# Performance work log

Hardware: AMD Instinct MI355X
Metric: run time of the kernel (lower is better)

## Reference

```python
import jax, jax.numpy as jnp
import numpy as np

EMBED = 512
HEADS = 8
DIM_HEAD = 64          # embed_dim // 8
LANDMARKS = 256        # embed_dim // 2
PINV_ITERS = 6
RES_K = 33             # nystrom residual_conv_kernel default
SCALE = DIM_HEAD ** -0.5


def layer_norm(x, g, b, eps=1e-5):
    mu = x.mean(-1, keepdims=True)
    var = ((x - mu) ** 2).mean(-1, keepdims=True)
    return (x - mu) / jnp.sqrt(var + eps) * g + b


def moore_penrose_pinv(x, iters=PINV_ITERS):
    # iterative Moore-Penrose pseudo-inverse (lucidrains nystrom-attention)
    ax = jnp.abs(x)
    z = jnp.swapaxes(x, -1, -2) / (ax.sum(-1).max() * ax.sum(-2).max())
    I = jnp.eye(x.shape[-1], dtype=x.dtype)
    for _ in range(iters):
        xz = x @ z
        z = 0.25 * z @ (13. * I - xz @ (15. * I - xz @ (7. * I - xz)))
    return z


def nystrom_attention(x, w_qkv, w_out, b_out, res_k):
    b, n, _ = x.shape
    m = LANDMARKS
    pad = (m - n % m) % m
    xp = jnp.pad(x, ((0, 0), (pad, 0), (0, 0)))  # left-pad like F.pad(..., padding, 0)
    np_ = n + pad
    qkv = (xp @ w_qkv).reshape(b, np_, 3, HEADS, DIM_HEAD)
    q = qkv[:, :, 0].transpose(0, 2, 1, 3) * SCALE   # [b,h,np,dh]
    k = qkv[:, :, 1].transpose(0, 2, 1, 3)
    v = qkv[:, :, 2].transpose(0, 2, 1, 3)
    l = np_ // m
    q_l = q.reshape(b, HEADS, m, l, DIM_HEAD).mean(3)  # [b,h,m,dh]
    k_l = k.reshape(b, HEADS, m, l, DIM_HEAD).mean(3)
    attn1 = jax.nn.softmax(jnp.einsum('bhid,bhjd->bhij', q, k_l), -1)    # [b,h,np,m]
    attn2 = jax.nn.softmax(jnp.einsum('bhid,bhjd->bhij', q_l, k_l), -1)  # [b,h,m,m]
    attn3 = jax.nn.softmax(jnp.einsum('bhid,bhjd->bhij', q_l, k), -1)    # [b,h,m,np]
    out = (attn1 @ moore_penrose_pinv(attn2)) @ (attn3 @ v)              # [b,h,np,dh]
    # depthwise residual conv over the sequence dim, per head (shared across dh)
    v_c = v.transpose(0, 3, 1, 2).reshape(b * DIM_HEAD, HEADS, np_)
    res = jax.lax.conv_general_dilated(
        v_c, res_k[:, None, :], (1,), [(RES_K // 2, RES_K // 2)],
        dimension_numbers=('NCH', 'OIH', 'NCH'), feature_group_count=HEADS)
    out = out + res.reshape(b, DIM_HEAD, HEADS, np_).transpose(0, 2, 3, 1)
    out = out.transpose(0, 2, 1, 3).reshape(b, np_, HEADS * DIM_HEAD)
    out = out @ w_out + b_out
    return out[:, -n:]  # drop left padding


def dwconv2d(x, w, b, k):
    # x: [B,C,H,W], w: [C,1,k,k] depthwise
    y = jax.lax.conv_general_dilated(
        x, w, (1, 1), [(k // 2, k // 2)] * 2,
        dimension_numbers=('NCHW', 'OIHW', 'NCHW'), feature_group_count=x.shape[1])
    return y + b[None, :, None, None]


def ppeg(x, H, W, w7, b7, w5, b5, w3, b3):
    B, _, C = x.shape
    cls_tok, feat = x[:, :1], x[:, 1:]
    f = feat.transpose(0, 2, 1).reshape(B, C, H, W)
    y = f + dwconv2d(f, w7, b7, 7) + dwconv2d(f, w5, b5, 5) + dwconv2d(f, w3, b3, 3)
    y = y.reshape(B, C, H * W).transpose(0, 2, 1)
    return jnp.concatenate([cls_tok, y], axis=1)


def reference(h, w_fc1, b_fc1, cls_token,
              ln1_g, ln1_b, qkv1_w, out1_w, out1_b, res1_k,
              conv7_w, conv7_b, conv5_w, conv5_b, conv3_w, conv3_b,
              ln2_g, ln2_b, qkv2_w, out2_w, out2_b, res2_k,
              lnf_g, lnf_b):
    h = jax.nn.relu(h @ w_fc1 + b_fc1)                 # [B,N,512]
    B, N, C = h.shape
    _H = int(np.ceil(np.sqrt(N)))
    add = _H * _H - N
    h = jnp.concatenate([h, h[:, :add]], axis=1)       # square padding
    h = jnp.concatenate([jnp.broadcast_to(cls_token, (B, 1, C)), h], axis=1)
    h = h + nystrom_attention(layer_norm(h, ln1_g, ln1_b), qkv1_w, out1_w, out1_b, res1_k)
    h = ppeg(h, _H, _H, conv7_w, conv7_b, conv5_w, conv5_b, conv3_w, conv3_b)
    h = h + nystrom_attention(layer_norm(h, ln2_g, ln2_b), qkv2_w, out2_w, out2_b, res2_k)
    return layer_norm(h, lnf_g, lnf_b)[:, 0]           # [B,512]


def setup_inputs() -> dict:
    key = jax.random.key(0)
    ks = jax.random.split(key, 24)
    B, N, IN_DIM = 2, 4096, 1024
    w = lambda k, shape, s=0.02: jax.random.normal(k, shape, jnp.float32) * s
    z = lambda shape: jnp.zeros(shape, jnp.float32)
    o = lambda shape: jnp.ones(shape, jnp.float32)
    return {
        'h': jax.random.normal(ks[0], (B, N, IN_DIM), jnp.float32),
        'w_fc1': w(ks[1], (IN_DIM, EMBED)), 'b_fc1': z((EMBED,)),
        'cls_token': w(ks[2], (1, 1, EMBED)),
        'ln1_g': o((EMBED,)), 'ln1_b': z((EMBED,)),
        'qkv1_w': w(ks[3], (EMBED, 3 * HEADS * DIM_HEAD)),
        'out1_w': w(ks[4], (HEADS * DIM_HEAD, EMBED)), 'out1_b': z((EMBED,)),
        'res1_k': w(ks[5], (HEADS, RES_K), 0.1),
        'conv7_w': w(ks[6], (EMBED, 1, 7, 7), 0.05), 'conv7_b': z((EMBED,)),
        'conv5_w': w(ks[7], (EMBED, 1, 5, 5), 0.05), 'conv5_b': z((EMBED,)),
        'conv3_w': w(ks[8], (EMBED, 1, 3, 3), 0.05), 'conv3_b': z((EMBED,)),
        'ln2_g': o((EMBED,)), 'ln2_b': z((EMBED,)),
        'qkv2_w': w(ks[9], (EMBED, 3 * HEADS * DIM_HEAD)),
        'out2_w': w(ks[10], (HEADS * DIM_HEAD, EMBED)), 'out2_b': z((EMBED,)),
        'res2_k': w(ks[11], (HEADS, RES_K), 0.1),
        'lnf_g': o((EMBED,)), 'lnf_b': z((EMBED,)),
    }
```

## Files before the change

### kernel.cpp

```cpp
#include <hip/hip_runtime.h>
#include <hip/hip_bf16.h>

#define HEADS 8
#define DH 64
#define EMB 512
#define NP 4352
#define NTOK 4097
#define PADF 255
#define LM 256
#define SCALE 0.125f

typedef __attribute__((ext_vector_type(8))) short bf8;
typedef __attribute__((ext_vector_type(4))) float f4;
typedef __attribute__((ext_vector_type(8))) unsigned short us8;
typedef __attribute__((ext_vector_type(4))) unsigned short us4;
typedef unsigned short u16;

__device__ __forceinline__ u16 f2b(float f){
  union { float f; unsigned u; } x; x.f = f;
  unsigned r = x.u + 0x7fffu + ((x.u>>16)&1u);
  return (u16)(r>>16);
}
__device__ __forceinline__ float b2f(u16 h){
  union { unsigned u; float f; } x; x.u = ((unsigned)h)<<16;
  return x.f;
}

__device__ __forceinline__ void gload_lds(const u16* g, u16* l){
  __builtin_amdgcn_global_load_lds((const __attribute__((address_space(1))) void*)g,
                                   (__attribute__((address_space(3))) void*)l, 16, 0, 0);
}

template<int MODE>
__global__ __launch_bounds__(256)
void k_g128(const u16* __restrict__ A, const u16* __restrict__ B,
            float* __restrict__ C, u16* __restrict__ C16,
            int K, int lda, int ldb, int ldc,
            long sAb, long sAh, long sBb, long sBh, long sCb, long sCh, int nh,
            float alpha, const float* __restrict__ bias, int relu, int rowoff,
            int nx, int ksplit)
{
  int z = blockIdx.z;
  const u16* Ab = A + (long)(z/nh)*sAb + (long)(z%nh)*sAh;
  const u16* Bb = B + (long)(z/nh)*sBb + (long)(z%nh)*sBh;
  long cb = (long)(z/nh)*sCb + (long)(z%nh)*sCh;
  int bx = blockIdx.x % nx, kc = blockIdx.x / nx;
  int m0 = blockIdx.y*128, n0 = bx*128;
  int klen = K/ksplit, kbeg = kc*klen, nch = klen/32;
  __shared__ u16 As[2][4096];
  __shared__ u16 Bs[2][4096];
  int tid=threadIdx.x, w=tid>>6, lane=tid&63, q=lane>>4, lr=lane&15;
  int wrow=(w>>1)*64, wcol=(w&1)*64;
  int srow = tid>>2, scol = (tid&3)*8;
  const u16* ga  = Ab + (long)(m0+srow)*lda + kbeg + scol;
  const u16* ga2 = Ab + (long)(m0+64+srow)*lda + kbeg + scol;
  const u16* gb  = Bb + (long)(n0+srow)*ldb + kbeg + scol;
  const u16* gb2 = Bb + (long)(n0+64+srow)*ldb + kbeg + scol;
  int lo = srow*32 + scol;
  f4 acc[4][4] = {};
  auto stage = [&](int r, int c){
    gload_lds(ga  + c*32, &As[r][lo]);
    gload_lds(ga2 + c*32, &As[r][2048+lo]);
    gload_lds(gb  + c*32, &Bs[r][lo]);
    gload_lds(gb2 + c*32, &Bs[r][2048+lo]);
  };
  auto compute = [&](int r){
    bf8 af[4], bfr[4];
    #pragma unroll
    for(int rr=0;rr<4;rr++) af[rr]  = *(const bf8*)&As[r][(wrow + rr*16 + lr)*32 + q*8];
    #pragma unroll
    for(int t=0;t<4;t++) bfr[t] = *(const bf8*)&Bs[r][(wcol + t*16 + lr)*32 + q*8];
    #pragma unroll
    for(int rr=0;rr<4;rr++)
      #pragma unroll
      for(int t=0;t<4;t++)
        acc[rr][t] = __builtin_amdgcn_mfma_f32_16x16x32_bf16(af[rr], bfr[t], acc[rr][t], 0,0,0);
  };
  stage(0,0);
  __syncthreads();
  for(int c=1;c<nch;c++){
    stage(c&1, c);
    compute((c-1)&1);
    __syncthreads();
  }
  compute((nch-1)&1);
  #pragma unroll
  for(int r=0;r<4;r++){
    #pragma unroll
    for(int t=0;t<4;t++){
      #pragma unroll
      for(int e=0;e<4;e++){
        int gm = m0 + wrow + r*16 + q*4 + e;
        int gn = n0 + wcol + t*16 + lr;
        float v = acc[r][t][e]*alpha;
        if(MODE==4){
          if(bias && kc==0) v += bias[gn];
          if(gm>=rowoff) atomicAdd(&C[cb + (long)(gm-rowoff)*ldc + gn], v);
        } else {
          if(bias) v += bias[gn];
          if(relu) v = fmaxf(v,0.f);
          if(MODE==0) C[cb + (long)gm*ldc + gn] = v;
          else if(MODE==2) C16[cb + (long)gm*ldc + gn] = f2b(v);
          else { if(gm>=rowoff) C[cb + (long)(gm-rowoff)*ldc + gn] += v; }
        }
      }
    }
  }
}

template<int MODE>
__global__ __launch_bounds__(256)
void k_g64(const u16* __restrict__ A, const u16* __restrict__ B,
           float* __restrict__ C, u16* __restrict__ C16,
           int K, int lda, int ldb, int ldc,
           long sAb, long sAh, long sBb, long sBh, long sCb, long sCh, int nh,
           float alpha, const float* __restrict__ bias, int rowoff, int moff,
           int nx, int ksplit)
{
  int z = blockIdx.z;
  const u16* Ab = A + (long)(z/nh)*sAb + (long)(z%nh)*sAh;
  const u16* Bb = B + (long)(z/nh)*sBb + (long)(z%nh)*sBh;
  long cb = (long)(z/nh)*sCb + (long)(z%nh)*sCh;
  int bx = blockIdx.x % nx, kc = blockIdx.x / nx;
  int m0 = blockIdx.y*64 + moff, n0 = bx*64;
  int klen = K/ksplit, kbeg = kc*klen, nch = klen/32;
  __shared__ u16 As[2][2048];
  __shared__ u16 Bs[2][2048];
  int tid=threadIdx.x, w=tid>>6, lane=tid&63, q=lane>>4, lr=lane&15;
  int srow = tid>>2, scol = (tid&3)*8;
  const u16* ga = Ab + (long)(m0+srow)*lda + kbeg + scol;
  const u16* gb = Bb + (long)(n0+srow)*ldb + kbeg + scol;
  int lo = srow*32 + scol;
  f4 acc[4] = {};
  auto stage = [&](int r, int c){
    gload_lds(ga + c*32, &As[r][lo]);
    gload_lds(gb + c*32, &Bs[r][lo]);
  };
  auto compute = [&](int r){
    bf8 af = *(const bf8*)&As[r][(w*16 + lr)*32 + q*8];
    #pragma unroll
    for(int t=0;t<4;t++){
      bf8 bfr = *(const bf8*)&Bs[r][(t*16 + lr)*32 + q*8];
      acc[t] = __builtin_amdgcn_mfma_f32_16x16x32_bf16(af, bfr, acc[t], 0,0,0);
    }
  };
  stage(0,0);
  __syncthreads();
  for(int c=1;c<nch;c++){
    stage(c&1, c);
    compute((c-1)&1);
    __syncthreads();
  }
  compute((nch-1)&1);
  #pragma unroll
  for(int t=0;t<4;t++){
    #pragma unroll
    for(int e=0;e<4;e++){
      int gm = m0 + w*16 + q*4 + e;
      int gn = n0 + t*16 + lr;
      float v = acc[t][e]*alpha;
      if(MODE==0) C[cb + (long)gm*ldc + gn] = v;
      else if(MODE==2) C16[cb + (long)gm*ldc + gn] = f2b(v);
      else if(MODE==3) atomicAdd(&C[cb + (long)gm*ldc + gn], v);
      else if(MODE==5){
        v += bias[gn];
        if(gm>=rowoff) C[cb + (long)(gm-rowoff)*ldc + gn] += v;
      }
    }
  }
}

__global__ __launch_bounds__(256)
void k_pg3(const u16* __restrict__ Ah, const u16* __restrict__ Al,
           const u16* __restrict__ Bh, const u16* __restrict__ Bl,
           u16* __restrict__ Oh, u16* __restrict__ Ol, float na, float nd,
           u16* __restrict__ TOh, u16* __restrict__ TOl, float ta, float td)
{
  long zo = (long)blockIdx.z*65536;
  int m0 = blockIdx.y*32, n0 = blockIdx.x*64;
  __shared__ u16 S[2][6144];
  int tid=threadIdx.x, w=tid>>6, lane=tid&63, q=lane>>4, lr=lane&15;
  int t2 = tid & 127;
  const u16* srcA = (tid<128 ? Ah : Al) + zo + (long)(m0 + (t2>>2))*256 + (t2&3)*8;
  const u16* srcBh = Bh + zo + (long)(n0 + (tid>>2))*256 + (tid&3)*8;
  const u16* srcBl = Bl + zo + (long)(n0 + (tid>>2))*256 + (tid&3)*8;
  f4 acc[2] = {};
  auto stage = [&](int r, int c){
    gload_lds(srcA  + c*32, &S[r][tid*8]);
    gload_lds(srcBh + c*32, &S[r][2048 + tid*8]);
    gload_lds(srcBl + c*32, &S[r][4096 + tid*8]);
  };
  int mrow = (w>>1)*16 + lr;
  auto compute = [&](int r){
    bf8 ah = *(const bf8*)&S[r][mrow*32 + q*8];
    bf8 al = *(const bf8*)&S[r][1024 + mrow*32 + q*8];
    #pragma unroll
    for(int t=0;t<2;t++){
      int nrow = (w&1)*32 + t*16 + lr;
      bf8 bh = *(const bf8*)&S[r][2048 + nrow*32 + q*8];
      bf8 bl = *(const bf8*)&S[r][4096 + nrow*32 + q*8];
      acc[t] = __builtin_amdgcn_mfma_f32_16x16x32_bf16(ah, bh, acc[t], 0,0,0);
      acc[t] = __builtin_amdgcn_mfma_f32_16x16x32_bf16(ah, bl, acc[t], 0,0,0);
      acc[t] = __builtin_amdgcn_mfma_f32_16x16x32_bf16(al, bh, acc[t], 0,0,0);
    }
  };
  stage(0,0);
  __syncthreads();
  #pragma unroll
  for(int c=1;c<8;c++){
    stage(c&1, c);
    compute((c-1)&1);
    __syncthreads();
  }
  compute(1);
  #pragma unroll
  for(int t=0;t<2;t++){
    int gn = n0 + (w&1)*32 + t*16 + lr;
    if(Oh){
      #pragma unroll
      for(int r=0;r<4;r++){
        int gm = m0 + (w>>1)*16 + q*4 + r;
        float v = na*acc[t][r] + ((gm==gn)?nd:0.f);
        u16 h = f2b(v);
        long o = zo + (long)gm*256 + gn;
        Oh[o] = h; Ol[o] = f2b(v - b2f(h));
      }
    }
    if(TOh){
      us4 th, tl;
      #pragma unroll
      for(int r=0;r<4;r++){
        int gm = m0 + (w>>1)*16 + q*4 + r;
        float v = ta*acc[t][r] + ((gm==gn)?td:0.f);
        u16 h = f2b(v);
        th[r] = h; tl[r] = f2b(v - b2f(h));
      }
      long o = zo + (long)gn*256 + (m0 + (w>>1)*16 + q*4);
      *(us4*)&TOh[o] = th; *(us4*)&TOl[o] = tl;
    }
  }
}

__global__ __launch_bounds__(128)
void k_att3(const u16* __restrict__ qkv16, const u16* __restrict__ ql,
            const u16* __restrict__ vT, float* __restrict__ partO,
            float* __restrict__ pm, float* __restrict__ pl)
{
  int kc = blockIdx.x, jt = blockIdx.y, z = blockIdx.z;
  int b = z>>3, h = z&7;
  __shared__ u16 SQ[32*64];
  __shared__ u16 SK[2][64*64];
  __shared__ u16 SV[2][64*64];
  __shared__ u16 SP[32*64];
  int tid=threadIdx.x, w=tid>>6, lane=tid&63, q=lane>>4, lr=lane&15;
  const u16* kb = qkv16 + (long)b*NP*1536 + 512 + h*64;
  const u16* vb = vT + (long)z*64*NP;
  int t00 = kc*1088;
  {
    const u16* qb = ql + (long)z*16384 + jt*32*64;
    #pragma unroll
    for(int p=0;p<2;p++){ int idx = tid + p*128; gload_lds(qb + idx*8, &SQ[idx*8]); }
  }
  auto stageKV = [&](int r, int i){
    int t0 = t00 + i*64;
    #pragma unroll
    for(int p=0;p<4;p++){
      int idx = tid + p*128; int row = idx>>3, c8 = (idx&7)*8;
      gload_lds(kb + (long)(t0+row)*1536 + c8, &SK[r][idx*8]);
      gload_lds(vb + (long)row*NP + t0 + c8, &SV[r][idx*8]);
    }
  };
  stageKV(0,0);
  __syncthreads();
  bf8 af0 = *(const bf8*)&SQ[(w*16+lr)*64 + q*8];
  bf8 af1 = *(const bf8*)&SQ[(w*16+lr)*64 + 32 + q*8];
  f4 o[4] = {};
  float m[4] = {-3e38f,-3e38f,-3e38f,-3e38f};
  float l[4] = {0.f,0.f,0.f,0.f};
  for(int i=0;i<17;i++){
    int cur = i&1;
    if(i<16) stageKV(cur^1, i+1);
    f4 s[4] = {};
    #pragma unroll
    for(int t=0;t<4;t++){
      bf8 b0 = *(const bf8*)&SK[cur][(t*16+lr)*64 + q*8];
      bf8 b1 = *(const bf8*)&SK[cur][(t*16+lr)*64 + 32 + q*8];
      s[t] = __builtin_amdgcn_mfma_f32_16x16x32_bf16(af0, b0, s[t], 0,0,0);
      s[t] = __builtin_amdgcn_mfma_f32_16x16x32_bf16(af1, b1, s[t], 0,0,0);
    }
    float tm[4];
    #pragma unroll
    for(int e=0;e<4;e++) tm[e] = fmaxf(fmaxf(s[0][e],s[1][e]), fmaxf(s[2][e],s[3][e]));
    #pragma unroll
    for(int sh=1; sh<16; sh<<=1)
      #pragma unroll
      for(int e=0;e<4;e++) tm[e] = fmaxf(tm[e], __shfl_xor(tm[e], sh));
    float rs[4];
    #pragma unroll
    for(int e=0;e<4;e++){
      float mn = fmaxf(m[e], tm[e]);
      float sc = expf(m[e]-mn);
      m[e] = mn;
      l[e] *= sc;
      rs[e] = 0.f;
      o[0][e]*=sc; o[1][e]*=sc; o[2][e]*=sc; o[3][e]*=sc;
    }
    #pragma unroll
    for(int t=0;t<4;t++)
      #pragma unroll
      for(int e=0;e<4;e++){
        float p = expf(s[t][e]-m[e]);
        rs[e] += p;
        SP[(w*16+q*4+e)*64 + t*16+lr] = f2b(p);
      }
    #pragma unroll
    for(int sh=1; sh<16; sh<<=1)
      #pragma unroll
      for(int e=0;e<4;e++) rs[e] += __shfl_xor(rs[e], sh);
    #pragma unroll
    for(int e=0;e<4;e++) l[e] += rs[e];
    #pragma unroll
    for(int ks=0;ks<2;ks++){
      bf8 pa = *(const bf8*)&SP[(w*16+lr)*64 + ks*32 + q*8];
      #pragma unroll
      for(int t2=0;t2<4;t2++){
        bf8 vv = *(const bf8*)&SV[cur][(t2*16+lr)*64 + ks*32 + q*8];
        o[t2] = __builtin_amdgcn_mfma_f32_16x16x32_bf16(pa, vv, o[t2], 0,0,0);
      }
    }
    __syncthreads();
  }
  long pb = (long)(z*4+kc)*256 + jt*32 + w*16;
  #pragma unroll
  for(int e=0;e<4;e++){
    int jg = q*4+e;
    #pragma unroll
    for(int t2=0;t2<4;t2++)
      partO[(pb + jg)*64 + t2*16 + lr] = o[t2][e];
    if(lr==0){ pm[pb + jg] = m[e]; pl[pb + jg] = l[e]; }
  }
}

__global__ __launch_bounds__(128)
void k_mrg3(const float* __restrict__ partO, const float* __restrict__ pm,
            const float* __restrict__ pl, u16* __restrict__ avbT16)
{
  int jq = blockIdx.x, z = blockIdx.y, tid = threadIdx.x;
  __shared__ float wk[64][4];
  __shared__ u16 T[64][66];
  if(tid < 64){
    int j = jq*64 + tid;
    float mm[4], ll[4];
    #pragma unroll
    for(int kc=0;kc<4;kc++){ mm[kc]=pm[(z*4+kc)*256 + j]; ll[kc]=pl[(z*4+kc)*256 + j]; }
    float M = fmaxf(fmaxf(mm[0],mm[1]),fmaxf(mm[2],mm[3]));
    float e0=expf(mm[0]-M), e1=expf(mm[1]-M), e2=expf(mm[2]-M), e3=expf(mm[3]-M);
    float inv = 1.f/(ll[0]*e0+ll[1]*e1+ll[2]*e2+ll[3]*e3);
    wk[tid][0]=e0*inv; wk[tid][1]=e1*inv; wk[tid][2]=e2*inv; wk[tid][3]=e3*inv;
  }
  __syncthreads();
  float acc[32];
  #pragma unroll
  for(int p=0;p<32;p++) acc[p]=0.f;
  for(int kc=0;kc<4;kc++){
    long base = ((long)(z*4+kc)*256 + jq*64)*64;
    #pragma unroll
    for(int p=0;p<32;p++){
      int idx = tid + p*128;
      acc[p] += wk[idx>>6][kc]*partO[base + idx];
    }
  }
  #pragma unroll
  for(int p=0;p<32;p++){ int idx = tid + p*128; T[idx&63][idx>>6] = f2b(acc[p]); }
  __syncthreads();
  int d = tid>>1, jh = (tid&1)*32;
  u16* dst = avbT16 + (long)(z*64+d)*256 + jq*64 + jh;
  #pragma unroll
  for(int c=0;c<4;c++){
    us8 vv;
    #pragma unroll
    for(int u=0;u<8;u++) vv[u] = T[d][jh + c*8 + u];
    *(us8*)&dst[c*8] = vv;
  }
}

__global__ __launch_bounds__(256)
void k_att1(const u16* __restrict__ qkv16, const u16* __restrict__ kl,
            const u16* __restrict__ zavT, float* __restrict__ Qc)
{
  int z = blockIdx.y, b = z>>3, h = z&7;
  int m0 = blockIdx.x*64;
  __shared__ u16 SQ[64*64];
  __shared__ u16 SKL[256*64];
  __shared__ u16 SZV[64*256];
  int tid=threadIdx.x, w=tid>>6, lane=tid&63, q=lane>>4, lr=lane&15;
  {
    const u16* qb = qkv16 + (long)b*NP*1536 + h*64;
    #pragma unroll
    for(int p=0;p<2;p++){
      int idx = tid + p*256; int row = idx>>3, c8 = (idx&7)*8;
      gload_lds(qb + (long)(m0+row)*1536 + c8, &SQ[row*64 + c8]);
    }
    const u16* kb = kl + (long)z*16384;
    #pragma unroll
    for(int p=0;p<8;p++){
      int idx = tid + p*256; int row = idx>>3, c8 = (idx&7)*8;
      gload_lds(kb + row*64 + c8, &SKL[row*64 + c8]);
    }
    const u16* zb = zavT + (long)z*16384;
    #pragma unroll
    for(int p=0;p<8;p++){
      int idx = tid + p*256; int row = idx>>5, c8 = (idx&31)*8;
      gload_lds(zb + row*256 + c8, &SZV[row*256 + c8]);
    }
  }
  __syncthreads();
  f4 acc[16] = {};
  {
    bf8 af0 = *(const bf8*)&SQ[(w*16+lr)*64 + q*8];
    bf8 af1 = *(const bf8*)&SQ[(w*16+lr)*64 + 32 + q*8];
    #pragma unroll
    for(int t=0;t<16;t++){
      bf8 b0 = *(const bf8*)&SKL[(t*16+lr)*64 + q*8];
      bf8 b1 = *(const bf8*)&SKL[(t*16+lr)*64 + 32 + q*8];
      acc[t] = __builtin_amdgcn_mfma_f32_16x16x32_bf16(af0, b0, acc[t], 0,0,0);
      acc[t] = __builtin_amdgcn_mfma_f32_16x16x32_bf16(af1, b1, acc[t], 0,0,0);
    }
  }
  float mx[4] = {-1e30f,-1e30f,-1e30f,-1e30f};
  #pragma unroll
  for(int t=0;t<16;t++)
    #pragma unroll
    for(int e=0;e<4;e++) mx[e] = fmaxf(mx[e], acc[t][e]*SCALE);
  #pragma unroll
  for(int s=1;s<16;s<<=1)
    #pragma unroll
    for(int e=0;e<4;e++) mx[e] = fmaxf(mx[e], __shfl_xor(mx[e], s));
  float sm[4] = {0.f,0.f,0.f,0.f};
  #pragma unroll
  for(int t=0;t<16;t++)
    #pragma unroll
    for(int e=0;e<4;e++){ float p = expf(acc[t][e]*SCALE - mx[e]); acc[t][e]=p; sm[e]+=p; }
  #pragma unroll
  for(int s=1;s<16;s<<=1)
    #pragma unroll
    for(int e=0;e<4;e++) sm[e] += __shfl_xor(sm[e], s);
  float inv[4];
  #pragma unroll
  for(int e=0;e<4;e++) inv[e] = 1.f/sm[e];
  __syncthreads();
  u16* PS = SKL;
  #pragma unroll
  for(int t=0;t<16;t++)
    #pragma unroll
    for(int e=0;e<4;e++)
      PS[(w*16 + q*4 + e)*256 + t*16 + lr] = f2b(acc[t][e]*inv[e]);
  __syncthreads();
  f4 acc2[4] = {};
  #pragma unroll
  for(int ks=0;ks<8;ks++){
    bf8 af = *(const bf8*)&PS[(w*16+lr)*256 + ks*32 + q*8];
    #pragma unroll
    for(int t=0;t<4;t++){
      bf8 bf_ = *(const bf8*)&SZV[(t*16+lr)*256 + ks*32 + q*8];
      acc2[t] = __builtin_amdgcn_mfma_f32_16x16x32_bf16(af, bf_, acc2[t], 0,0,0);
    }
  }
  #pragma unroll
  for(int t=0;t<4;t++)
    #pragma unroll
    for(int r=0;r<4;r++){
      int gm = m0 + w*16 + q*4 + r;
      int gd = t*16 + lr;
      Qc[((long)b*NP + gm)*512 + h*64 + gd] = acc2[t][r];
    }
}

__global__ __launch_bounds__(256)
void k_smw32(float* __restrict__ X){
  long row = (long)blockIdx.x*4 + (threadIdx.x>>6);
  int lane = threadIdx.x & 63;
  float* p = X + row*256;
  float4 v = *(float4*)&p[lane*4];
  float m = fmaxf(fmaxf(v.x,v.y),fmaxf(v.z,v.w));
  for(int s=32;s;s>>=1) m = fmaxf(m, __shfl_xor(m, s));
  float e0=expf(v.x-m), e1=expf(v.y-m), e2=expf(v.z-m), e3=expf(v.w-m);
  float sum = e0+e1+e2+e3;
  for(int s=32;s;s>>=1) sum += __shfl_xor(sum, s);
  float inv = 1.f/sum;
  float4 o = {e0*inv, e1*inv, e2*inv, e3*inv};
  *(float4*)&p[lane*4] = o;
}

__global__ void k_wT(const float* __restrict__ in, u16* __restrict__ out, int K, int N){
  int n0=blockIdx.x*32, k0=blockIdx.y*32, tid=threadIdx.x;
  __shared__ float T[32][33];
  int lr=tid&31, lc=tid>>5;
  #pragma unroll
  for(int p=0;p<4;p++) T[lc+8*p][lr] = in[(long)(k0+lc+8*p)*N + n0+lr];
  __syncthreads();
  #pragma unroll
  for(int p=0;p<4;p++) out[(long)(n0+lc+8*p)*K + k0+lr] = f2b(T[lr][lc+8*p]);
}

__global__ __launch_bounds__(256)
void k_vT(const u16* __restrict__ qkv16, u16* __restrict__ vT){
  int t0=blockIdx.x*64, h=blockIdx.y, b=blockIdx.z, tid=threadIdx.x;
  __shared__ u16 T[64][72];
  const u16* src = qkv16 + (long)b*NP*1536 + 1024 + h*64;
  for(int s=0;s<2;s++){
    int idx=tid+s*256; int row=idx>>3, c8=(idx&7)*8;
    *(us8*)&T[row][c8] = *(const us8*)&src[(long)(t0+row)*1536 + c8];
  }
  __syncthreads();
  u16* dst = vT + ((long)(b*8+h)*64)*NP;
  int d = tid>>2, j0=(tid&3)*16;
  us8 v0,v1;
  #pragma unroll
  for(int jj=0;jj<8;jj++){ v0[jj]=T[j0+jj][d]; v1[jj]=T[j0+8+jj][d]; }
  *(us8*)&dst[(long)d*NP + t0 + j0]     = v0;
  *(us8*)&dst[(long)d*NP + t0 + j0 + 8] = v1;
}

__global__ void k_cvt16(const float* __restrict__ in, u16* __restrict__ out, long n){
  long i = (long)blockIdx.x*256 + threadIdx.x;
  if(i<n) out[i] = f2b(in[i]);
}

__global__ void k_cls(const float* __restrict__ cls, float* __restrict__ seq){
  int b = blockIdx.x;
  seq[(long)b*NTOK*EMB + threadIdx.x] = cls[threadIdx.x];
}

__global__ void k_ln_pad(const float* __restrict__ seq, u16* __restrict__ xp,
                         const float* __restrict__ g, const float* __restrict__ bb){
  int b = blockIdx.y, i = blockIdx.x, tid = threadIdx.x;
  u16* out = xp + ((long)b*NP + i)*EMB;
  if(i < PADF){ out[tid]=0; out[tid+256]=0; return; }
  const float* x = seq + ((long)b*NTOK + (i-PADF))*EMB;
  float v0 = x[tid], v1 = x[tid+256];
  __shared__ float red[256];
  red[tid]=v0+v1; __syncthreads();
  for(int s=128;s>0;s>>=1){ if(tid<s) red[tid]+=red[tid+s]; __syncthreads(); }
  float mu = red[0]*(1.0f/512.0f); __syncthreads();
  float d0=v0-mu, d1=v1-mu;
  red[tid]=d0*d0+d1*d1; __syncthreads();
  for(int s=128;s>0;s>>=1){ if(tid<s) red[tid]+=red[tid+s]; __syncthreads(); }
  float rstd = rsqrtf(red[0]*(1.0f/512.0f) + 1e-5f);
  out[tid]     = f2b(d0*rstd*g[tid]     + bb[tid]);
  out[tid+256] = f2b(d1*rstd*g[tid+256] + bb[tid+256]);
}

__global__ void k_landmarks(const u16* __restrict__ qkv, u16* __restrict__ q_l, u16* __restrict__ k_l){
  int j = blockIdx.x, h = blockIdx.y, b = blockIdx.z, d = threadIdx.x;
  const u16* base = qkv + (long)b*NP*1536 + h*64 + d;
  float sq=0.f, sk=0.f;
  for(int l=0;l<17;l++){
    long row = (long)(j*17+l)*1536;
    sq += b2f(base[row]);
    sk += b2f(base[row+512]);
  }
  long o = (((long)b*HEADS + h)*LM + j)*DH + d;
  q_l[o] = f2b(sq * (SCALE/17.0f));
  k_l[o] = f2b(sk * (1.0f/17.0f));
}

__global__ void k_pinv_norm(const float* __restrict__ A2, float* __restrict__ rmax, float* __restrict__ cmax){
  int z = blockIdx.x, tid = threadIdx.x;
  const float* X = A2 + (long)z*65536;
  float rs=0.f, cs=0.f;
  for(int j=0;j<256;j++){ rs += fabsf(X[tid*256+j]); cs += fabsf(X[j*256+tid]); }
  __shared__ float r1[256], r2[256];
  r1[tid]=rs; r2[tid]=cs; __syncthreads();
  for(int s=128;s>0;s>>=1){ if(tid<s){ r1[tid]=fmaxf(r1[tid],r1[tid+s]); r2[tid]=fmaxf(r2[tid],r2[tid+s]); } __syncthreads(); }
  if(tid==0){ rmax[z]=r1[0]; cmax[z]=r2[0]; }
}

__global__ void k_pair_init(const float* __restrict__ att2,
    const float* __restrict__ rmax, const float* __restrict__ cmax,
    u16* __restrict__ Xh, u16* __restrict__ Xl,
    u16* __restrict__ Zh, u16* __restrict__ Zl,
    u16* __restrict__ Zth, u16* __restrict__ Ztl)
{
  long zo = (long)blockIdx.z*65536;
  int i0 = blockIdx.y*64, j0 = blockIdx.x*64;
  float rm=0.f, cm=0.f;
  for(int t=0;t<16;t++){ rm=fmaxf(rm,rmax[t]); cm=fmaxf(cm,cmax[t]); }
  float inv = 1.0f/(rm*cm);
  __shared__ float T[64][68];
  int tid = threadIdx.x;
  int li = tid>>2, jc = (tid&3)*16;
  #pragma unroll
  for(int u=0;u<4;u++){
    float4 v = *(const float4*)&att2[zo + (long)(i0+li)*256 + j0 + jc + u*4];
    T[li][jc+u*4]=v.x; T[li][jc+u*4+1]=v.y; T[li][jc+u*4+2]=v.z; T[li][jc+u*4+3]=v.w;
    long o = zo + (long)(i0+li)*256 + j0 + jc + u*4;
    float vv[4] = {v.x,v.y,v.z,v.w};
    us4 xh, xl, zth, ztl;
    #pragma unroll
    for(int c=0;c<4;c++){
      u16 h = f2b(vv[c]); xh[c]=h; xl[c]=f2b(vv[c]-b2f(h));
      float zt = vv[c]*inv;
      u16 h2 = f2b(zt); zth[c]=h2; ztl[c]=f2b(zt-b2f(h2));
    }
    *(us4*)&Xh[o]=xh; *(us4*)&Xl[o]=xl; *(us4*)&Zth[o]=zth; *(us4*)&Ztl[o]=ztl;
  }
  __syncthreads();
  int lj = tid>>2, ic = (tid&3)*16;
  #pragma unroll
  for(int r=0;r<16;r++){
    float x = T[ic+r][lj]*inv;
    u16 h = f2b(x);
    long o = zo + (long)(j0+lj)*256 + i0 + ic + r;
    Zh[o]=h; Zl[o]=f2b(x-b2f(h));
  }
}

__global__ __launch_bounds__(256)
void k_rconv(const u16* __restrict__ qkv16, const float* __restrict__ resk,
             const float* __restrict__ Qin, u16* __restrict__ Qo16){
  int t0 = blockIdx.x*64, h = blockIdx.y, b = blockIdx.z;
  __shared__ float V[96*64];
  const u16* vb = qkv16 + (long)b*NP*1536 + 1024 + h*64;
  int tid = threadIdx.x;
  #pragma unroll
  for(int s=0;s<3;s++){
    int idx = tid + s*256;
    int row = idx>>3, c8 = (idx&7)*8;
    int p = t0 - 16 + row;
    if(p>=0 && p<NP){
      us8 v = *(const us8*)&vb[(long)p*1536 + c8];
      #pragma unroll
      for(int jj=0;jj<8;jj++) V[row*64+c8+jj] = b2f(v[jj]);
    } else {
      #pragma unroll
      for(int jj=0;jj<8;jj++) V[row*64+c8+jj] = 0.f;
    }
  }
  __syncthreads();
  int d = tid&63, lt = (tid>>6)*16;
  float acc[16] = {};
  #pragma unroll
  for(int s=0;s<48;s++){
    float val = V[(lt+s)*64 + d];
    #pragma unroll
    for(int j=0;j<16;j++){
      int tap = s - j;
      if(tap>=0 && tap<33) acc[j] += resk[h*33+tap]*val;
    }
  }
  #pragma unroll
  for(int j=0;j<16;j++){
    long idx = ((long)b*NP + t0 + lt + j)*EMB + h*64 + d;
    Qo16[idx] = f2b(Qin[idx] + acc[j]);
  }
}

__global__ __launch_bounds__(256)
void k_ppeg(const float* __restrict__ seq, float* __restrict__ out,
    const float* __restrict__ w7,const float* __restrict__ b7,
    const float* __restrict__ w5,const float* __restrict__ b5,
    const float* __restrict__ w3,const float* __restrict__ b3){
  int b = blockIdx.z, cg = blockIdx.y;
  int rp = blockIdx.x>>1, xs = blockIdx.x&1;
  int ch0 = cg*64;
  __shared__ float s7[64*49], s5[64*25], s3[64*9], sbias[64];
  int tid = threadIdx.x;
  for(int i=tid;i<64*49;i+=256) s7[i] = w7[ch0*49+i];
  for(int i=tid;i<64*25;i+=256) s5[i] = w5[ch0*25+i];
  for(int i=tid;i<64*9;i+=256)  s3[i] = w3[ch0*9+i];
  if(tid<64) sbias[tid] = b7[ch0+tid]+b5[ch0+tid]+b3[ch0+tid];
  if(cg==0 && blockIdx.x==0){
    out[(long)b*NTOK*EMB + tid]       = seq[(long)b*NTOK*EMB + tid];
    out[(long)b*NTOK*EMB + 256 + tid] = seq[(long)b*NTOK*EMB + 256 + tid];
  }
  __syncthreads();
  int c = tid & 63;
  int y = rp*4 + (tid>>6);
  const float* sbase = seq + (long)b*NTOK*EMB + EMB + (ch0 + c);
  float* obase = out + (long)b*NTOK*EMB + EMB + (ch0 + c);
  const float* W7 = &s7[c*49];
  const float* W5 = &s5[c*25];
  const float* W3 = &s3[c*9];
  float bsum = sbias[c];
  for(int xc=0;xc<4;xc++){
    int xb = xs*32 + xc*8;
    float acc[8];
    #pragma unroll
    for(int j=0;j<8;j++) acc[j] = sbase[(long)(y*64+xb+j)*EMB] + bsum;
    #pragma unroll
    for(int dy=-3;dy<=3;dy++){
      int yy = y+dy;
      if(yy<0||yy>=64) continue;
      float v[14];
      #pragma unroll
      for(int u=0;u<14;u++){
        int xx = xb + u - 3;
        v[u] = (xx>=0 && xx<64) ? sbase[(long)(yy*64+xx)*EMB] : 0.f;
      }
      #pragma unroll
      for(int dx=-3;dx<=3;dx++){
        float wsum = W7[(dy+3)*7+(dx+3)];
        if(dy>=-2&&dy<=2&&dx>=-2&&dx<=2) wsum += W5[(dy+2)*5+(dx+2)];
        if(dy>=-1&&dy<=1&&dx>=-1&&dx<=1) wsum += W3[(dy+1)*3+(dx+1)];
        #pragma unroll
        for(int j=0;j<8;j++) acc[j] += v[j+dx+3]*wsum;
      }
    }
    #pragma unroll
    for(int j=0;j<8;j++) obase[(long)(y*64+xb+j)*EMB] = acc[j];
  }
}

__global__ void k_final_ln(const float* __restrict__ seq, const float* __restrict__ g,
                           const float* __restrict__ bb, float* __restrict__ out){
  int b = blockIdx.x, tid = threadIdx.x;
  const float* x = seq + (long)b*NTOK*EMB;
  float v0 = x[tid], v1 = x[tid+256];
  __shared__ float red[256];
  red[tid]=v0+v1; __syncthreads();
  for(int s=128;s>0;s>>=1){ if(tid<s) red[tid]+=red[tid+s]; __syncthreads(); }
  float mu = red[0]*(1.0f/512.0f); __syncthreads();
  float d0=v0-mu, d1=v1-mu;
  red[tid]=d0*d0+d1*d1; __syncthreads();
  for(int s=128;s>0;s>>=1){ if(tid<s) red[tid]+=red[tid+s]; __syncthreads(); }
  float rstd = rsqrtf(red[0]*(1.0f/512.0f) + 1e-5f);
  out[b*512+tid]     = d0*rstd*g[tid]     + bb[tid];
  out[b*512+tid+256] = d1*rstd*g[tid+256] + bb[tid+256];
}

extern "C" void kernel_launch(void* const* d_in, const int* in_sizes, int n_in,
                              void* d_out, int out_size, void* d_ws, size_t ws_size,
                              hipStream_t stream) {
  const float* in[24];
  for(int i=0;i<24;i++) in[i] = (const float*)d_in[i];

  float* W = (float*)d_ws;
  size_t off = 0;
  float* seqA = W+off; off += 4195328;
  float* seqB = W+off; off += 4195328;
  float* att2 = W+off; off += 1048576;
  float* Qc   = W+off; off += 4456448;
  float* partO= W+off; off += 1048576;
  float* pm   = W+off; off += 16384;
  float* pl   = W+off; off += 16384;
  u16* xpb    = (u16*)(W+off); off += 2228224;
  u16* qkvb16 = (u16*)(W+off); off += 6684672;
  u16* vT16   = (u16*)(W+off); off += 2228224;
  u16* q_l16  = (u16*)(W+off); off += 131072;
  u16* k_l16  = (u16*)(W+off); off += 131072;
  u16* avbT16 = (u16*)(W+off); off += 131072;
  u16* zavT16 = (u16*)(W+off); off += 131072;
  u16* Qc16   = (u16*)(W+off); off += 2228224;
  u16* qkvwT1 = (u16*)(W+off); off += 393216;
  u16* qkvwT2 = (u16*)(W+off); off += 393216;
  u16* outwT1 = (u16*)(W+off); off += 131072;
  u16* outwT2 = (u16*)(W+off); off += 131072;
  u16* pairs  = (u16*)(W+off); off += 9437184;
  float* rmax = W+off; off += 16;
  float* cmax = W+off; off += 16;
  if (ws_size < off*sizeof(float)) return;

  u16* h16   = pairs;
  u16* wfc1T = pairs + 8388608;

  const long PB = 1048576;
  u16 *Xh=pairs, *Xl=pairs+PB;
  u16 *Z0h=pairs+2*PB, *Z0l=pairs+3*PB, *Z0th=pairs+4*PB, *Z0tl=pairs+5*PB;
  u16 *Z1h=pairs+6*PB, *Z1l=pairs+7*PB, *Z1th=pairs+8*PB, *Z1tl=pairs+9*PB;
  u16 *Ph=pairs+10*PB, *Pl=pairs+11*PB;
  u16 *Tth=pairs+12*PB, *Ttl=pairs+13*PB;
  u16 *Uth=pairs+14*PB, *Utl=pairs+15*PB;
  u16 *Vth=pairs+16*PB, *Vtl=pairs+17*PB;

  k_cvt16<<<32768,256,0,stream>>>(in[0], h16, 8388608L);
  k_wT<<<dim3(16,32),256,0,stream>>>(in[1],  wfc1T, 1024, 512);
  k_wT<<<dim3(48,16),256,0,stream>>>(in[6],  qkvwT1, 512, 1536);
  k_wT<<<dim3(48,16),256,0,stream>>>(in[18], qkvwT2, 512, 1536);
  k_wT<<<dim3(16,16),256,0,stream>>>(in[7],  outwT1, 512, 512);
  k_wT<<<dim3(16,16),256,0,stream>>>(in[19], outwT2, 512, 512);

  k_g128<0><<<dim3(4,32,2),256,0,stream>>>(h16, wfc1T, seqA+EMB, nullptr,
      1024, 1024,1024,512, 4194304L,0, 0,0, (long)NTOK*EMB,0, 1, 1.0f, in[2], 1, 0, 4, 1);
  k_cls<<<2,512,0,stream>>>(in[3], seqA);

  auto attention = [&](float* seq, const float* lng,const float* lnb,
                       const u16* qkvwT, const u16* outwT, const float* outb, const float* resk){
    k_ln_pad<<<dim3(NP,2),256,0,stream>>>(seq, xpb, lng, lnb);
    k_g128<2><<<dim3(12,34,2),256,0,stream>>>(xpb, qkvwT, nullptr, qkvb16,
        512, 512,512,1536, (long)NP*512,0, 0,0, (long)NP*1536,0, 1, 1.0f, nullptr, 0, 0, 12, 1);
    k_landmarks<<<dim3(LM,HEADS,2),64,0,stream>>>(qkvb16, q_l16, k_l16);
    k_vT<<<dim3(68,8,2),256,0,stream>>>(qkvb16, vT16);
    k_g128<0><<<dim3(2,2,16),256,0,stream>>>(q_l16, k_l16, att2, nullptr,
        64, 64,64,256, 0,16384, 0,16384, 0,65536, 16, 1.0f, nullptr, 0, 0, 2, 1);
    k_smw32<<<1024,256,0,stream>>>(att2);
    k_pinv_norm<<<16,256,0,stream>>>(att2, rmax, cmax);
    k_pair_init<<<dim3(4,4,16),256,0,stream>>>(att2, rmax, cmax, Xh,Xl, Z0h,Z0l, Z0th,Z0tl);
    dim3 pgrid(4,8,16);
    for(int it=0; it<6; it++){
      u16 *Zh_=(it&1)?Z1h:Z0h, *Zl_=(it&1)?Z1l:Z0l, *Zth_=(it&1)?Z1th:Z0th, *Ztl_=(it&1)?Z1tl:Z0tl;
      u16 *Nh_=(it&1)?Z0h:Z1h, *Nl_=(it&1)?Z0l:Z1l, *Nth_=(it&1)?Z0th:Z1th, *Ntl_=(it&1)?Z0tl:Z1tl;
      k_pg3<<<pgrid,256,0,stream>>>(Xh,Xl, Zth_,Ztl_, Ph,Pl,1.0f,0.f, Tth,Ttl,-1.0f,7.f);
      k_pg3<<<pgrid,256,0,stream>>>(Ph,Pl, Tth,Ttl, nullptr,nullptr,0.f,0.f, Uth,Utl,-1.0f,15.f);
      k_pg3<<<pgrid,256,0,stream>>>(Ph,Pl, Uth,Utl, nullptr,nullptr,0.f,0.f, Vth,Vtl,-1.0f,13.f);
      if(it<5) k_pg3<<<pgrid,256,0,stream>>>(Zh_,Zl_, Vth,Vtl, Nh_,Nl_,0.25f,0.f, Nth_,Ntl_,0.25f,0.f);
      else     k_pg3<<<pgrid,256,0,stream>>>(Zh_,Zl_, Vth,Vtl, Nh_,Nl_,0.25f,0.f, nullptr,nullptr,0.f,0.f);
    }
    k_att3<<<dim3(4,8,16),128,0,stream>>>(qkvb16, q_l16, vT16, partO, pm, pl);
    k_mrg3<<<dim3(4,16),128,0,stream>>>(partO, pm, pl, avbT16);
    k_g64<2><<<dim3(4,1,16),256,0,stream>>>(avbT16, Z0h, nullptr, zavT16,
        256, 256,256,256, 0,16384L, 0,65536L, 0,16384L, 16, 1.0f, nullptr, 0, 0, 4, 1);
    k_att1<<<dim3(68,16),256,0,stream>>>(qkvb16, k_l16, zavT16, Qc);
    k_rconv<<<dim3(68,8,2),256,0,stream>>>(qkvb16, resk, Qc, Qc16);
    k_g64<5><<<dim3(8,65,2),256,0,stream>>>(Qc16, outwT, seq, nullptr,
        512, 512,512,512, (long)NP*512,0, 0,0, (long)NTOK*EMB,0, 1, 1.0f, outb, PADF, 192, 8, 1);
  };

  attention(seqA, in[4], in[5], qkvwT1, outwT1, in[8], in[9]);
  k_ppeg<<<dim3(32,8,2),256,0,stream>>>(seqA, seqB, in[10],in[11],in[12],in[13],in[14],in[15]);
  attention(seqB, in[16], in[17], qkvwT2, outwT2, in[20], in[21]);
  k_final_ln<<<2,256,0,stream>>>(seqB, in[22], in[23], (float*)d_out);
}
```

Before: 1.025 ms.

## Split attn3 into more key chunks, widen blocks, swizzle LDS

The landmark-to-token attention (attn3 @ v) now splits the 4352-token key dimension into 17 chunks of 256 instead of 4 chunks of 1088. Each block processes 64 query landmarks with 256 threads instead of 32 with 128, giving 1088 blocks instead of 512 and a much shorter serial loop per block. LDS tiles for Q, K, V and P use an XOR swizzle on 8-element groups to avoid bank conflicts. The merge kernel is rewritten to combine 17 partial softmax results with finer 16-row tiles, at the cost of a much larger partial-output buffer and more merge traffic.

```diff
diff --git a/kernel.cpp b/kernel.cpp
--- a/kernel.cpp
+++ b/kernel.cpp
@@ -241,50 +241,55 @@
   }
 }
 
-__global__ __launch_bounds__(128)
+__global__ __launch_bounds__(256)
 void k_att3(const u16* __restrict__ qkv16, const u16* __restrict__ ql,
             const u16* __restrict__ vT, float* __restrict__ partO,
             float* __restrict__ pm, float* __restrict__ pl)
 {
   int kc = blockIdx.x, jt = blockIdx.y, z = blockIdx.z;
   int b = z>>3, h = z&7;
-  __shared__ u16 SQ[32*64];
+  __shared__ u16 SQ[64*64];
   __shared__ u16 SK[2][64*64];
   __shared__ u16 SV[2][64*64];
-  __shared__ u16 SP[32*64];
+  __shared__ u16 SP[64*64];
   int tid=threadIdx.x, w=tid>>6, lane=tid&63, q=lane>>4, lr=lane&15;
   const u16* kb = qkv16 + (long)b*NP*1536 + 512 + h*64;
   const u16* vb = vT + (long)z*64*NP;
-  int t00 = kc*1088;
+  int t00 = kc*256;
   {
-    const u16* qb = ql + (long)z*16384 + jt*32*64;
-    #pragma unroll
-    for(int p=0;p<2;p++){ int idx = tid + p*128; gload_lds(qb + idx*8, &SQ[idx*8]); }
+    const u16* qb = ql + (long)z*16384 + jt*64*64;
+    #pragma unroll
+    for(int p=0;p<2;p++){
+      int idx = tid + p*256; int row = idx>>3; int js = ((idx&7)^(row&7))<<3;
+      gload_lds(qb + row*64 + js, &SQ[idx*8]);
+    }
   }
   auto stageKV = [&](int r, int i){
     int t0 = t00 + i*64;
     #pragma unroll
-    for(int p=0;p<4;p++){
-      int idx = tid + p*128; int row = idx>>3, c8 = (idx&7)*8;
-      gload_lds(kb + (long)(t0+row)*1536 + c8, &SK[r][idx*8]);
-      gload_lds(vb + (long)row*NP + t0 + c8, &SV[r][idx*8]);
+    for(int p=0;p<2;p++){
+      int idx = tid + p*256; int row = idx>>3; int js = ((idx&7)^(row&7))<<3;
+      gload_lds(kb + (long)(t0+row)*1536 + js, &SK[r][idx*8]);
+      gload_lds(vb + (long)row*NP + t0 + js, &SV[r][idx*8]);
     }
   };
   stageKV(0,0);
   __syncthreads();
-  bf8 af0 = *(const bf8*)&SQ[(w*16+lr)*64 + q*8];
-  bf8 af1 = *(const bf8*)&SQ[(w*16+lr)*64 + 32 + q*8];
+  int ar = w*16+lr;
+  bf8 af0 = *(const bf8*)&SQ[ar*64 + ((q^(ar&7))<<3)];
+  bf8 af1 = *(const bf8*)&SQ[ar*64 + (((q|4)^(ar&7))<<3)];
   f4 o[4] = {};
   float m[4] = {-3e38f,-3e38f,-3e38f,-3e38f};
   float l[4] = {0.f,0.f,0.f,0.f};
-  for(int i=0;i<17;i++){
+  for(int i=0;i<4;i++){
     int cur = i&1;
-    if(i<16) stageKV(cur^1, i+1);
+    if(i<3) stageKV(cur^1, i+1);
     f4 s[4] = {};
     #pragma unroll
     for(int t=0;t<4;t++){
-      bf8 b0 = *(const bf8*)&SK[cur][(t*16+lr)*64 + q*8];
-      bf8 b1 = *(const bf8*)&SK[cur][(t*16+lr)*64 + 32 + q*8];
+      int br = t*16+lr;
+      bf8 b0 = *(const bf8*)&SK[cur][br*64 + ((q^(br&7))<<3)];
+      bf8 b1 = *(const bf8*)&SK[cur][br*64 + (((q|4)^(br&7))<<3)];
       s[t] = __builtin_amdgcn_mfma_f32_16x16x32_bf16(af0, b0, s[t], 0,0,0);
       s[t] = __builtin_amdgcn_mfma_f32_16x16x32_bf16(af1, b1, s[t], 0,0,0);
     }
@@ -311,7 +316,8 @@
       for(int e=0;e<4;e++){
         float p = expf(s[t][e]-m[e]);
         rs[e] += p;
-        SP[(w*16+q*4+e)*64 + t*16+lr] = f2b(p);
+        int prow = w*16+q*4+e, pcol = t*16+lr;
+        SP[prow*64 + (((pcol>>3)^(prow&7))<<3) + (pcol&7)] = f2b(p);
       }
     #pragma unroll
     for(int sh=1; sh<16; sh<<=1)
@@ -319,18 +325,20 @@
       for(int e=0;e<4;e++) rs[e] += __shfl_xor(rs[e], sh);
     #pragma unroll
     for(int e=0;e<4;e++) l[e] += rs[e];
+    int pr = w*16+lr;
     #pragma unroll
     for(int ks=0;ks<2;ks++){
-      bf8 pa = *(const bf8*)&SP[(w*16+lr)*64 + ks*32 + q*8];
+      bf8 pa = *(const bf8*)&SP[pr*64 + (((ks*4+q)^(pr&7))<<3)];
       #pragma unroll
       for(int t2=0;t2<4;t2++){
-        bf8 vv = *(const bf8*)&SV[cur][(t2*16+lr)*64 + ks*32 + q*8];
+        int rr = t2*16+lr;
+        bf8 vv = *(const bf8*)&SV[cur][rr*64 + (((ks*4+q)^(rr&7))<<3)];
         o[t2] = __builtin_amdgcn_mfma_f32_16x16x32_bf16(pa, vv, o[t2], 0,0,0);
       }
     }
     __syncthreads();
   }
-  long pb = (long)(z*4+kc)*256 + jt*32 + w*16;
+  long pb = (long)(z*17+kc)*256 + jt*64 + w*16;
   #pragma unroll
   for(int e=0;e<4;e++){
     int jg = q*4+e;
@@ -346,42 +354,42 @@
             const float* __restrict__ pl, u16* __restrict__ avbT16)
 {
   int jq = blockIdx.x, z = blockIdx.y, tid = threadIdx.x;
-  __shared__ float wk[64][4];
-  __shared__ u16 T[64][66];
-  if(tid < 64){
-    int j = jq*64 + tid;
-    float mm[4], ll[4];
-    #pragma unroll
-    for(int kc=0;kc<4;kc++){ mm[kc]=pm[(z*4+kc)*256 + j]; ll[kc]=pl[(z*4+kc)*256 + j]; }
-    float M = fmaxf(fmaxf(mm[0],mm[1]),fmaxf(mm[2],mm[3]));
-    float e0=expf(mm[0]-M), e1=expf(mm[1]-M), e2=expf(mm[2]-M), e3=expf(mm[3]-M);
-    float inv = 1.f/(ll[0]*e0+ll[1]*e1+ll[2]*e2+ll[3]*e3);
-    wk[tid][0]=e0*inv; wk[tid][1]=e1*inv; wk[tid][2]=e2*inv; wk[tid][3]=e3*inv;
-  }
-  __syncthreads();
-  float acc[32];
-  #pragma unroll
-  for(int p=0;p<32;p++) acc[p]=0.f;
-  for(int kc=0;kc<4;kc++){
-    long base = ((long)(z*4+kc)*256 + jq*64)*64;
-    #pragma unroll
-    for(int p=0;p<32;p++){
+  int j0 = jq*16;
+  __shared__ float wk[16][17];
+  __shared__ u16 T[16][72];
+  if(tid < 16){
+    int j = j0 + tid;
+    float mm[17];
+    float M = -3e38f;
+    #pragma unroll
+    for(int kc=0;kc<17;kc++){ mm[kc]=pm[(z*17+kc)*256 + j]; M=fmaxf(M,mm[kc]); }
+    float s = 0.f;
+    #pragma unroll
+    for(int kc=0;kc<17;kc++){ float e=expf(mm[kc]-M); wk[tid][kc]=e; s+=e*pl[(z*17+kc)*256 + j]; }
+    float inv = 1.f/s;
+    #pragma unroll
+    for(int kc=0;kc<17;kc++) wk[tid][kc]*=inv;
+  }
+  __syncthreads();
+  float acc[8];
+  #pragma unroll
+  for(int p=0;p<8;p++) acc[p]=0.f;
+  for(int kc=0;kc<17;kc++){
+    long base = ((long)(z*17+kc)*256 + j0)*64;
+    #pragma unroll
+    for(int p=0;p<8;p++){
       int idx = tid + p*128;
       acc[p] += wk[idx>>6][kc]*partO[base + idx];
     }
   }
   #pragma unroll
-  for(int p=0;p<32;p++){ int idx = tid + p*128; T[idx&63][idx>>6] = f2b(acc[p]); }
-  __syncthreads();
-  int d = tid>>1, jh = (tid&1)*32;
-  u16* dst = avbT16 + (long)(z*64+d)*256 + jq*64 + jh;
-  #pragma unroll
-  for(int c=0;c<4;c++){
-    us8 vv;
-    #pragma unroll
-    for(int u=0;u<8;u++) vv[u] = T[d][jh + c*8 + u];
-    *(us8*)&dst[c*8] = vv;
-  }
+  for(int p=0;p<8;p++){ int idx = tid + p*128; T[idx>>6][idx&63] = f2b(acc[p]); }
+  __syncthreads();
+  int d = tid>>1, jh = (tid&1)*8;
+  us8 vv;
+  #pragma unroll
+  for(int u=0;u<8;u++) vv[u] = T[jh+u][d];
+  *(us8*)&avbT16[(long)(z*64+d)*256 + j0 + jh] = vv;
 }
 
 __global__ __launch_bounds__(256)
@@ -741,9 +749,9 @@
   float* seqB = W+off; off += 4195328;
   float* att2 = W+off; off += 1048576;
   float* Qc   = W+off; off += 4456448;
-  float* partO= W+off; off += 1048576;
-  float* pm   = W+off; off += 16384;
-  float* pl   = W+off; off += 16384;
+  float* partO= W+off; off += 17825792;
+  float* pm   = W+off; off += 69632;
+  float* pl   = W+off; off += 69632;
   u16* xpb    = (u16*)(W+off); off += 2228224;
   u16* qkvb16 = (u16*)(W+off); off += 6684672;
   u16* vT16   = (u16*)(W+off); off += 2228224;
@@ -806,8 +814,8 @@
       if(it<5) k_pg3<<<pgrid,256,0,stream>>>(Zh_,Zl_, Vth,Vtl, Nh_,Nl_,0.25f,0.f, Nth_,Ntl_,0.25f,0.f);
       else     k_pg3<<<pgrid,256,0,stream>>>(Zh_,Zl_, Vth,Vtl, Nh_,Nl_,0.25f,0.f, nullptr,nullptr,0.f,0.f);
     }
-    k_att3<<<dim3(4,8,16),128,0,stream>>>(qkvb16, q_l16, vT16, partO, pm, pl);
-    k_mrg3<<<dim3(4,16),128,0,stream>>>(partO, pm, pl, avbT16);
+    k_att3<<<dim3(17,4,16),256,0,stream>>>(qkvb16, q_l16, vT16, partO, pm, pl);
+    k_mrg3<<<dim3(16,16),128,0,stream>>>(partO, pm, pl, avbT16);
     k_g64<2><<<dim3(4,1,16),256,0,stream>>>(avbT16, Z0h, nullptr, zavT16,
         256, 256,256,256, 0,16384L, 0,65536L, 0,16384L, 16, 1.0f, nullptr, 0, 0, 4, 1);
     k_att1<<<dim3(68,16),256,0,stream>>>(qkvb16, k_l16, zavT16, Qc);
```

New measurement: 986.9 us. 3.7% less time.
